# Kernel tuning notes

Hardware: AMD Instinct MI355X
Metric: run time of the kernel (lower is better)

Reference implementation:

```python
import jax, jax.numpy as jnp
import numpy as np

B, S1, S2, D1, D2, F = 8, 2048, 2048, 512, 512, 256

def setup_inputs() -> dict:
    key = jax.random.key(0)
    ks = jax.random.split(key, 10)
    sc1 = 1.0 / np.sqrt(D1)
    sc2 = 1.0 / np.sqrt(D2)
    scf = 1.0 / np.sqrt(F)
    return {
        "feat1": jax.random.normal(ks[0], (B, S1, D1), jnp.float32),
        "feat2": jax.random.normal(ks[1], (B, S2, D2), jnp.float32),
        "Wq": jax.random.normal(ks[2], (D1, F), jnp.float32) * sc1,
        "bq": jnp.zeros((F,), jnp.float32),
        "Wk": jax.random.normal(ks[3], (D2, F), jnp.float32) * sc2,
        "bk": jnp.zeros((F,), jnp.float32),
        "Wv": jax.random.normal(ks[4], (D2, F), jnp.float32) * sc2,
        "bv": jnp.zeros((F,), jnp.float32),
        "Wfc": jax.random.normal(ks[5], (F, F), jnp.float32) * scf,
        "bfc": jnp.zeros((F,), jnp.float32),
    }

def reference(feat1, feat2, Wq, bq, Wk, bk, Wv, bv, Wfc, bfc):
    Q = jnp.einsum('bsd,df->bsf', feat1, Wq) + bq          # [B,S1,F]
    K = jnp.einsum('btd,df->btf', feat2, Wk) + bk          # [B,S2,F]
    V = jnp.einsum('btd,df->btf', feat2, Wv) + bv          # [B,S2,F]
    scores = jnp.einsum('bsf,btf->bst', Q, K) / jnp.sqrt(jnp.float32(K.shape[-1]))
    attn = jax.nn.softmax(scores, axis=-1)                 # [B,S1,S2]
    attn_out = jnp.einsum('bst,btf->bsf', attn, V)         # [B,S1,F]
    out = jnp.einsum('bsf,fg->bsg', attn_out, Wfc) + bfc   # [B,S1,F]
    return out
```

## Files before the change

kernel.cpp:

```cpp
#include <hip/hip_runtime.h>
#include <hip/hip_bf16.h>

#define B_ 8
#define S1_ 2048
#define S2_ 2048
#define D_ 512
#define F_ 256

typedef __attribute__((ext_vector_type(4))) float f32x4;
typedef __attribute__((ext_vector_type(8))) short s16x8;
typedef __attribute__((ext_vector_type(4))) short s16x4;
typedef __attribute__((ext_vector_type(2))) int i32x2;

__device__ __forceinline__ short f2bf(float x) {
  union { float f; unsigned u; } v; v.f = x;
  unsigned r = v.u + 0x7fffu + ((v.u >> 16) & 1u);
  return (short)(r >> 16);
}

__device__ __forceinline__ int pk2bf(float a, float b) {
  union { __hip_bfloat162 h; int i; } u;
  u.h = __float22bfloat162_rn(make_float2(a, b));
  return u.i;
}

__global__ __launch_bounds__(256) void wtrans_kernel(
    const float* __restrict__ Wq, const float* __restrict__ Wk,
    const float* __restrict__ Wv, const float* __restrict__ Wfc,
    short* __restrict__ Wqt, short* __restrict__ Wkt,
    short* __restrict__ Wvt, short* __restrict__ Wfct) {
  int y = blockIdx.y;
  const float* W; short* Wt; int dl;
  if (y == 0)      { W = Wq;  Wt = Wqt;  dl = 9; }
  else if (y == 1) { W = Wk;  Wt = Wkt;  dl = 9; }
  else if (y == 2) { W = Wv;  Wt = Wvt;  dl = 9; }
  else             { W = Wfc; Wt = Wfct; dl = 8; }
  int idx = blockIdx.x * 256 + threadIdx.x;
  if (idx >= (F_ << dl)) return;
  int d = idx & ((1 << dl) - 1);
  int f = idx >> dl;
  Wt[idx] = f2bf(W[(size_t)d * F_ + f]);
}

__global__ __launch_bounds__(256) void proj_kernel(
    const float* __restrict__ feat1, const float* __restrict__ feat2,
    const short* __restrict__ Wqt, const short* __restrict__ Wkt,
    const short* __restrict__ Wvt,
    const float* __restrict__ bq, const float* __restrict__ bk,
    const float* __restrict__ bv,
    short* __restrict__ Qw, short* __restrict__ Kw, short* __restrict__ Vtw) {
  const float* A; const short* Wt; const float* bias; short* outp;
  float scale; int trans;
  if (blockIdx.z == 0)      { A = feat1; Wt = Wqt; bias = bq; outp = Qw;  scale = 0.0625f; trans = 0; }
  else if (blockIdx.z == 1) { A = feat2; Wt = Wkt; bias = bk; outp = Kw;  scale = 1.0f;    trans = 0; }
  else                      { A = feat2; Wt = Wvt; bias = bv; outp = Vtw; scale = 1.0f;    trans = 1; }

  __shared__ __align__(16) short As[128][72];
  __shared__ __align__(16) short Ws[128][72];

  int m0 = blockIdx.x * 128;
  int n0 = blockIdx.y * 128;
  int t = threadIdx.x;
  int w = t >> 6, L = t & 63, rowA = L & 15, quad = L >> 4;
  int wy = w >> 1, wx = w & 1;

  int srow = t >> 3, sc8 = (t & 7) * 8;

  f32x4 acc[4][4];
  for (int i = 0; i < 4; ++i)
    for (int j = 0; j < 4; ++j) acc[i][j] = (f32x4){0.f, 0.f, 0.f, 0.f};

  for (int k0 = 0; k0 < D_; k0 += 64) {
    for (int p = 0; p < 4; ++p) {
      int r = p * 32 + srow;
      const float* src = A + (size_t)(m0 + r) * D_ + k0 + sc8;
      f32x4 v0 = *(const f32x4*)src;
      f32x4 v1 = *(const f32x4*)(src + 4);
      s16x8 s;
      ((int*)&s)[0] = pk2bf(v0[0], v0[1]);
      ((int*)&s)[1] = pk2bf(v0[2], v0[3]);
      ((int*)&s)[2] = pk2bf(v1[0], v1[1]);
      ((int*)&s)[3] = pk2bf(v1[2], v1[3]);
      *(s16x8*)(&As[r][sc8]) = s;
    }
    for (int p = 0; p < 4; ++p) {
      int r = p * 32 + srow;
      *(s16x8*)(&Ws[r][sc8]) = *(const s16x8*)(Wt + (size_t)(n0 + r) * D_ + k0 + sc8);
    }
    __syncthreads();
    for (int kt = 0; kt < 2; ++kt) {
      s16x8 a[4];
      for (int mt = 0; mt < 4; ++mt)
        a[mt] = *(const s16x8*)(&As[wy * 64 + mt * 16 + rowA][kt * 32 + quad * 8]);
      for (int nt = 0; nt < 4; ++nt) {
        s16x8 b = *(const s16x8*)(&Ws[wx * 64 + nt * 16 + rowA][kt * 32 + quad * 8]);
        for (int mt = 0; mt < 4; ++mt)
          acc[mt][nt] = __builtin_amdgcn_mfma_f32_16x16x32_bf16(a[mt], b, acc[mt][nt], 0, 0, 0);
      }
    }
    __syncthreads();
  }

  if (!trans) {
    float bn[4];
    for (int nt = 0; nt < 4; ++nt) bn[nt] = bias[n0 + wx * 64 + nt * 16 + rowA];
    for (int mt = 0; mt < 4; ++mt) {
      int m = m0 + wy * 64 + mt * 16 + quad * 4;
      for (int nt = 0; nt < 4; ++nt) {
        int n = n0 + wx * 64 + nt * 16 + rowA;
        for (int r = 0; r < 4; ++r)
          outp[(size_t)(m + r) * F_ + n] = f2bf((acc[mt][nt][r] + bn[nt]) * scale);
      }
    }
  } else {
    int bb = m0 >> 11;
    int tbase = (m0 & (S2_ - 1)) + wy * 64;
    float bn[4];
    for (int nt = 0; nt < 4; ++nt) bn[nt] = bias[n0 + wx * 64 + nt * 16 + rowA];
    for (int nt = 0; nt < 4; ++nt) {
      int f = n0 + wx * 64 + nt * 16 + rowA;
      for (int mt = 0; mt < 4; ++mt) {
        int tt = tbase + mt * 16 + quad * 4;
        s16x4 o;
        for (int r = 0; r < 4; ++r) o[r] = f2bf(acc[mt][nt][r] + bn[nt]);
        *(s16x4*)(outp + ((size_t)bb * F_ + f) * S2_ + tt) = o;
      }
    }
  }
}

__global__ __launch_bounds__(512, 2) void flash_kernel(
    const short* __restrict__ Q,
    const short* __restrict__ K,
    const short* __restrict__ Vt,
    short* __restrict__ O) {
  __shared__ __align__(16) short Ks[2][64][264];
  __shared__ __align__(16) short Vs[2][256][72];
  __shared__ __align__(16) short Ps[4][16][72];

  int b = blockIdx.x >> 5;
  int s0 = (blockIdx.x & 31) * 64;
  int t = threadIdx.x;
  int w = t >> 6, L = t & 63, rowA = L & 15, quad = L >> 4;
  int rg = w & 3, ch = w >> 2;

  const short* Qb = Q + ((size_t)b * S1_ + s0 + rg * 16) * F_;
  const short* Kb = K + (size_t)b * S2_ * F_;
  const short* Vb = Vt + (size_t)b * F_ * S2_;

  int kr  = t >> 5;
  int kc8 = (t & 31) * 8;
  int vfb = t >> 3;
  int vc8 = (t & 7) * 8;

  s16x8 qf[8];
  for (int kt = 0; kt < 8; ++kt)
    qf[kt] = *(const s16x8*)(Qb + (size_t)rowA * F_ + kt * 32 + quad * 8);

  s16x8 kpre[4], vpre[4];
  for (int p = 0; p < 4; ++p) {
    kpre[p] = *(const s16x8*)(Kb + (size_t)(kr + p * 16) * F_ + kc8);
    vpre[p] = *(const s16x8*)(Vb + (size_t)(vfb + p * 64) * S2_ + vc8);
  }
  for (int p = 0; p < 4; ++p) {
    *(s16x8*)(&Ks[0][kr + p * 16][kc8]) = kpre[p];
    *(s16x8*)(&Vs[0][vfb + p * 64][vc8]) = vpre[p];
  }
  for (int p = 0; p < 4; ++p) {
    kpre[p] = *(const s16x8*)(Kb + (size_t)(64 + kr + p * 16) * F_ + kc8);
    vpre[p] = *(const s16x8*)(Vb + (size_t)(vfb + p * 64) * S2_ + 64 + vc8);
  }

  f32x4 o[8];
  for (int i = 0; i < 8; ++i) o[i] = (f32x4){0.f, 0.f, 0.f, 0.f};
  float l_lane[4] = {0.f, 0.f, 0.f, 0.f};

  for (int it = 0; it < 32; ++it) {
    int cb = it & 1;
    __syncthreads();
    if (it < 31) {
      for (int p = 0; p < 4; ++p) {
        *(s16x8*)(&Ks[1 - cb][kr + p * 16][kc8]) = kpre[p];
        *(s16x8*)(&Vs[1 - cb][vfb + p * 64][vc8]) = vpre[p];
      }
    }
    f32x4 s[2];
    s[0] = (f32x4){0.f, 0.f, 0.f, 0.f};
    s[1] = (f32x4){0.f, 0.f, 0.f, 0.f};
    for (int kt = 0; kt < 8; ++kt) {
      for (int n2 = 0; n2 < 2; ++n2) {
        s16x8 bfr = *(const s16x8*)(&Ks[cb][ch * 32 + n2 * 16 + rowA][kt * 32 + quad * 8]);
        s[n2] = __builtin_amdgcn_mfma_f32_16x16x32_bf16(qf[kt], bfr, s[n2], 0, 0, 0);
      }
    }
    for (int n2 = 0; n2 < 2; ++n2) {
      for (int r = 0; r < 4; ++r) {
        float p = __expf(s[n2][r]);
        l_lane[r] += p;
        Ps[rg][quad * 4 + r][ch * 32 + n2 * 16 + rowA] = f2bf(p);
      }
    }
    __syncthreads();
    if (it < 30) {
      int n0 = (it + 2) * 64;
      for (int p = 0; p < 4; ++p) {
        kpre[p] = *(const s16x8*)(Kb + (size_t)(n0 + kr + p * 16) * F_ + kc8);
        vpre[p] = *(const s16x8*)(Vb + (size_t)(vfb + p * 64) * S2_ + n0 + vc8);
      }
    }
    s16x8 pa0 = *(const s16x8*)(&Ps[rg][rowA][quad * 8]);
    s16x8 pa1 = *(const s16x8*)(&Ps[rg][rowA][32 + quad * 8]);
    for (int ft = 0; ft < 8; ++ft) {
      s16x8 v0 = *(const s16x8*)(&Vs[cb][ch * 128 + ft * 16 + rowA][quad * 8]);
      o[ft] = __builtin_amdgcn_mfma_f32_16x16x32_bf16(pa0, v0, o[ft], 0, 0, 0);
    }
    for (int ft = 0; ft < 8; ++ft) {
      s16x8 v1 = *(const s16x8*)(&Vs[cb][ch * 128 + ft * 16 + rowA][32 + quad * 8]);
      o[ft] = __builtin_amdgcn_mfma_f32_16x16x32_bf16(pa1, v1, o[ft], 0, 0, 0);
    }
  }

  float l[4];
  for (int r = 0; r < 4; ++r) {
    float x = l_lane[r];
    for (int off = 1; off < 16; off <<= 1)
      x += __shfl_xor(x, off, 64);
    l[r] = x;
  }
  __syncthreads();
  float* lf = (float*)&Ps[0][0][0];
  if (rowA == 0) {
    for (int r = 0; r < 4; ++r)
      lf[(rg * 16 + quad * 4 + r) * 2 + ch] = l[r];
  }
  __syncthreads();
  short* Ob = O + ((size_t)b * S1_ + s0 + rg * 16) * F_;
  for (int r = 0; r < 4; ++r) {
    int row = quad * 4 + r;
    float inv = 1.0f / (lf[(rg * 16 + row) * 2] + lf[(rg * 16 + row) * 2 + 1]);
    for (int ft = 0; ft < 8; ++ft)
      Ob[(size_t)row * F_ + ch * 128 + ft * 16 + rowA] = f2bf(o[ft][r] * inv);
  }
}

__global__ __launch_bounds__(256) void fc_kernel(
    const short* __restrict__ AO,
    const short* __restrict__ Wt,
    const float* __restrict__ bias,
    float* __restrict__ out) {
  __shared__ __align__(16) short As[128][72];
  __shared__ __align__(16) short Ws[128][72];

  int m0 = blockIdx.x * 128;
  int n0 = blockIdx.y * 128;
  int t = threadIdx.x;
  int w = t >> 6, L = t & 63, rowA = L & 15, quad = L >> 4;
  int wy = w >> 1, wx = w & 1;
  int srow = t >> 3, sc8 = (t & 7) * 8;

  f32x4 acc[4][4];
  for (int i = 0; i < 4; ++i)
    for (int j = 0; j < 4; ++j) acc[i][j] = (f32x4){0.f, 0.f, 0.f, 0.f};

  for (int k0 = 0; k0 < F_; k0 += 64) {
    for (int p = 0; p < 4; ++p) {
      int r = p * 32 + srow;
      *(s16x8*)(&As[r][sc8]) = *(const s16x8*)(AO + (size_t)(m0 + r) * F_ + k0 + sc8);
      *(s16x8*)(&Ws[r][sc8]) = *(const s16x8*)(Wt + (size_t)(n0 + r) * F_ + k0 + sc8);
    }
    __syncthreads();
    for (int kt = 0; kt < 2; ++kt) {
      s16x8 a[4];
      for (int mt = 0; mt < 4; ++mt)
        a[mt] = *(const s16x8*)(&As[wy * 64 + mt * 16 + rowA][kt * 32 + quad * 8]);
      for (int nt = 0; nt < 4; ++nt) {
        s16x8 b = *(const s16x8*)(&Ws[wx * 64 + nt * 16 + rowA][kt * 32 + quad * 8]);
        for (int mt = 0; mt < 4; ++mt)
          acc[mt][nt] = __builtin_amdgcn_mfma_f32_16x16x32_bf16(a[mt], b, acc[mt][nt], 0, 0, 0);
      }
    }
    __syncthreads();
  }

  float bn[4];
  for (int nt = 0; nt < 4; ++nt) bn[nt] = bias[n0 + wx * 64 + nt * 16 + rowA];
  for (int mt = 0; mt < 4; ++mt) {
    int m = m0 + wy * 64 + mt * 16 + quad * 4;
    for (int nt = 0; nt < 4; ++nt) {
      int n = n0 + wx * 64 + nt * 16 + rowA;
      for (int r = 0; r < 4; ++r)
        out[(size_t)(m + r) * F_ + n] = acc[mt][nt][r] + bn[nt];
    }
  }
}

extern "C" void kernel_launch(void* const* d_in, const int* in_sizes, int n_in,
                              void* d_out, int out_size, void* d_ws, size_t ws_size,
                              hipStream_t stream) {
  const float* feat1 = (const float*)d_in[0];
  const float* feat2 = (const float*)d_in[1];
  const float* Wq  = (const float*)d_in[2];
  const float* bq  = (const float*)d_in[3];
  const float* Wk  = (const float*)d_in[4];
  const float* bk  = (const float*)d_in[5];
  const float* Wv  = (const float*)d_in[6];
  const float* bv  = (const float*)d_in[7];
  const float* Wfc = (const float*)d_in[8];
  const float* bfc = (const float*)d_in[9];
  float* out = (float*)d_out;
  char* ws = (char*)d_ws;

  short* Qw   = (short*)(ws);
  short* Kw   = (short*)(ws + (size_t)(8u  << 20));
  short* Vtw  = (short*)(ws + (size_t)(16u << 20));
  short* AOw  = (short*)(ws + (size_t)(24u << 20));
  short* Wqt  = (short*)(ws + (size_t)(32u << 20));
  short* Wkt  = Wqt + 256 * 512;
  short* Wvt  = Wkt + 256 * 512;
  short* Wfct = Wvt + 256 * 512;

  wtrans_kernel<<<dim3(512, 4), 256, 0, stream>>>(Wq, Wk, Wv, Wfc, Wqt, Wkt, Wvt, Wfct);
  proj_kernel<<<dim3(128, 2, 3), 256, 0, stream>>>(feat1, feat2, Wqt, Wkt, Wvt,
                                                   bq, bk, bv, Qw, Kw, Vtw);
  flash_kernel<<<dim3(256), 512, 0, stream>>>(Qw, Kw, Vtw, AOw);
  fc_kernel<<<dim3(128, 2), 256, 0, stream>>>(AOw, Wfct, bfc, out);
}
```

Baseline: 220.0 us.

## Warp-specialize flash attention into score and PV waves; widen projection tiles

The flash kernel now splits its 8 waves into two roles. Four waves compute QK^T scores and the exp, writing P into a double-buffered shared tile. The other four waves do the P·V MFMAs one iteration behind, so score and output work overlap across the pipeline. K and V prefetch is restaged to match. Separately, the projection kernel uses 64x256 tiles so each block covers all of F and converts every fp32 activation row to bf16 only once, at the cost of a larger W tile in shared memory.

```diff
diff --git a/kernel.cpp b/kernel.cpp
--- a/kernel.cpp
+++ b/kernel.cpp
@@ -42,7 +42,7 @@
   Wt[idx] = f2bf(W[(size_t)d * F_ + f]);
 }
 
-__global__ __launch_bounds__(256) void proj_kernel(
+__global__ __launch_bounds__(256, 3) void proj_kernel(
     const float* __restrict__ feat1, const float* __restrict__ feat2,
     const short* __restrict__ Wqt, const short* __restrict__ Wkt,
     const short* __restrict__ Wvt,
@@ -51,51 +51,52 @@
     short* __restrict__ Qw, short* __restrict__ Kw, short* __restrict__ Vtw) {
   const float* A; const short* Wt; const float* bias; short* outp;
   float scale; int trans;
-  if (blockIdx.z == 0)      { A = feat1; Wt = Wqt; bias = bq; outp = Qw;  scale = 0.0625f; trans = 0; }
-  else if (blockIdx.z == 1) { A = feat2; Wt = Wkt; bias = bk; outp = Kw;  scale = 1.0f;    trans = 0; }
+  if (blockIdx.y == 0)      { A = feat1; Wt = Wqt; bias = bq; outp = Qw;  scale = 0.0625f; trans = 0; }
+  else if (blockIdx.y == 1) { A = feat2; Wt = Wkt; bias = bk; outp = Kw;  scale = 1.0f;    trans = 0; }
   else                      { A = feat2; Wt = Wvt; bias = bv; outp = Vtw; scale = 1.0f;    trans = 1; }
 
-  __shared__ __align__(16) short As[128][72];
-  __shared__ __align__(16) short Ws[128][72];
-
-  int m0 = blockIdx.x * 128;
-  int n0 = blockIdx.y * 128;
+  __shared__ __align__(16) short As[64][72];
+  __shared__ __align__(16) short Ws[256][72];
+
+  int m0 = blockIdx.x * 64;
   int t = threadIdx.x;
   int w = t >> 6, L = t & 63, rowA = L & 15, quad = L >> 4;
-  int wy = w >> 1, wx = w & 1;
-
-  int srow = t >> 3, sc8 = (t & 7) * 8;
+  int ar = t >> 2, ac16 = (t & 3) * 16;
 
   f32x4 acc[4][4];
   for (int i = 0; i < 4; ++i)
     for (int j = 0; j < 4; ++j) acc[i][j] = (f32x4){0.f, 0.f, 0.f, 0.f};
 
   for (int k0 = 0; k0 < D_; k0 += 64) {
+    {
+      const float* src = A + (size_t)(m0 + ar) * D_ + k0 + ac16;
+      f32x4 v0 = *(const f32x4*)(src);
+      f32x4 v1 = *(const f32x4*)(src + 4);
+      f32x4 v2 = *(const f32x4*)(src + 8);
+      f32x4 v3 = *(const f32x4*)(src + 12);
+      s16x8 s0, s1;
+      ((int*)&s0)[0] = pk2bf(v0[0], v0[1]); ((int*)&s0)[1] = pk2bf(v0[2], v0[3]);
+      ((int*)&s0)[2] = pk2bf(v1[0], v1[1]); ((int*)&s0)[3] = pk2bf(v1[2], v1[3]);
+      ((int*)&s1)[0] = pk2bf(v2[0], v2[1]); ((int*)&s1)[1] = pk2bf(v2[2], v2[3]);
+      ((int*)&s1)[2] = pk2bf(v3[0], v3[1]); ((int*)&s1)[3] = pk2bf(v3[2], v3[3]);
+      *(s16x8*)(&As[ar][ac16]) = s0;
+      *(s16x8*)(&As[ar][ac16 + 8]) = s1;
+    }
     for (int p = 0; p < 4; ++p) {
-      int r = p * 32 + srow;
-      const float* src = A + (size_t)(m0 + r) * D_ + k0 + sc8;
-      f32x4 v0 = *(const f32x4*)src;
-      f32x4 v1 = *(const f32x4*)(src + 4);
-      s16x8 s;
-      ((int*)&s)[0] = pk2bf(v0[0], v0[1]);
-      ((int*)&s)[1] = pk2bf(v0[2], v0[3]);
-      ((int*)&s)[2] = pk2bf(v1[0], v1[1]);
-      ((int*)&s)[3] = pk2bf(v1[2], v1[3]);
-      *(s16x8*)(&As[r][sc8]) = s;
-    }
-    for (int p = 0; p < 4; ++p) {
-      int r = p * 32 + srow;
-      *(s16x8*)(&Ws[r][sc8]) = *(const s16x8*)(Wt + (size_t)(n0 + r) * D_ + k0 + sc8);
+      int r = (t >> 2) + p * 64;
+      const short* src = Wt + (size_t)r * D_ + k0 + ac16;
+      *(s16x8*)(&Ws[r][ac16]) = *(const s16x8*)(src);
+      *(s16x8*)(&Ws[r][ac16 + 8]) = *(const s16x8*)(src + 8);
     }
     __syncthreads();
     for (int kt = 0; kt < 2; ++kt) {
       s16x8 a[4];
       for (int mt = 0; mt < 4; ++mt)
-        a[mt] = *(const s16x8*)(&As[wy * 64 + mt * 16 + rowA][kt * 32 + quad * 8]);
+        a[mt] = *(const s16x8*)(&As[mt * 16 + rowA][kt * 32 + quad * 8]);
       for (int nt = 0; nt < 4; ++nt) {
-        s16x8 b = *(const s16x8*)(&Ws[wx * 64 + nt * 16 + rowA][kt * 32 + quad * 8]);
+        s16x8 bfr = *(const s16x8*)(&Ws[w * 64 + nt * 16 + rowA][kt * 32 + quad * 8]);
         for (int mt = 0; mt < 4; ++mt)
-          acc[mt][nt] = __builtin_amdgcn_mfma_f32_16x16x32_bf16(a[mt], b, acc[mt][nt], 0, 0, 0);
+          acc[mt][nt] = __builtin_amdgcn_mfma_f32_16x16x32_bf16(a[mt], bfr, acc[mt][nt], 0, 0, 0);
       }
     }
     __syncthreads();
@@ -103,22 +104,22 @@
 
   if (!trans) {
     float bn[4];
-    for (int nt = 0; nt < 4; ++nt) bn[nt] = bias[n0 + wx * 64 + nt * 16 + rowA];
+    for (int nt = 0; nt < 4; ++nt) bn[nt] = bias[w * 64 + nt * 16 + rowA];
     for (int mt = 0; mt < 4; ++mt) {
-      int m = m0 + wy * 64 + mt * 16 + quad * 4;
+      int m = m0 + mt * 16 + quad * 4;
       for (int nt = 0; nt < 4; ++nt) {
-        int n = n0 + wx * 64 + nt * 16 + rowA;
+        int n = w * 64 + nt * 16 + rowA;
         for (int r = 0; r < 4; ++r)
           outp[(size_t)(m + r) * F_ + n] = f2bf((acc[mt][nt][r] + bn[nt]) * scale);
       }
     }
   } else {
     int bb = m0 >> 11;
-    int tbase = (m0 & (S2_ - 1)) + wy * 64;
+    int tbase = m0 & (S2_ - 1);
     float bn[4];
-    for (int nt = 0; nt < 4; ++nt) bn[nt] = bias[n0 + wx * 64 + nt * 16 + rowA];
+    for (int nt = 0; nt < 4; ++nt) bn[nt] = bias[w * 64 + nt * 16 + rowA];
     for (int nt = 0; nt < 4; ++nt) {
-      int f = n0 + wx * 64 + nt * 16 + rowA;
+      int f = w * 64 + nt * 16 + rowA;
       for (int mt = 0; mt < 4; ++mt) {
         int tt = tbase + mt * 16 + quad * 4;
         s16x4 o;
@@ -136,110 +137,123 @@
     short* __restrict__ O) {
   __shared__ __align__(16) short Ks[2][64][264];
   __shared__ __align__(16) short Vs[2][256][72];
-  __shared__ __align__(16) short Ps[4][16][72];
+  __shared__ __align__(16) short Ps[2][64][72];
 
   int b = blockIdx.x >> 5;
   int s0 = (blockIdx.x & 31) * 64;
   int t = threadIdx.x;
   int w = t >> 6, L = t & 63, rowA = L & 15, quad = L >> 4;
-  int rg = w & 3, ch = w >> 2;
-
-  const short* Qb = Q + ((size_t)b * S1_ + s0 + rg * 16) * F_;
+  int isS = (w < 4);
+
   const short* Kb = K + (size_t)b * S2_ * F_;
   const short* Vb = Vt + (size_t)b * F_ * S2_;
 
-  int kr  = t >> 5;
-  int kc8 = (t & 31) * 8;
-  int vfb = t >> 3;
-  int vc8 = (t & 7) * 8;
-
-  s16x8 qf[8];
-  for (int kt = 0; kt < 8; ++kt)
-    qf[kt] = *(const s16x8*)(Qb + (size_t)rowA * F_ + kt * 32 + quad * 8);
+  int kr = t >> 5, kc8 = (t & 31) * 8;
+  int vr = t >> 3, vc8 = (t & 7) * 8;
+
+  int rs = (w & 1) * 32, cs = ((w >> 1) & 1) * 32;
+  int mg = (w - 4) & 1, fg = ((w - 4) >> 1) & 1;
+
+  s16x8 qf[2][8];
+  if (isS) {
+    const short* Qb = Q + ((size_t)b * S1_ + s0 + rs) * F_;
+    for (int mt = 0; mt < 2; ++mt)
+      for (int kt = 0; kt < 8; ++kt)
+        qf[mt][kt] = *(const s16x8*)(Qb + (size_t)(mt * 16 + rowA) * F_ + kt * 32 + quad * 8);
+  }
+  f32x4 o[2][8];
+  for (int i = 0; i < 2; ++i)
+    for (int j = 0; j < 8; ++j) o[i][j] = (f32x4){0.f, 0.f, 0.f, 0.f};
+  float l_lane[2][4] = {{0.f,0.f,0.f,0.f},{0.f,0.f,0.f,0.f}};
 
   s16x8 kpre[4], vpre[4];
-  for (int p = 0; p < 4; ++p) {
+  for (int p = 0; p < 4; ++p)
     kpre[p] = *(const s16x8*)(Kb + (size_t)(kr + p * 16) * F_ + kc8);
-    vpre[p] = *(const s16x8*)(Vb + (size_t)(vfb + p * 64) * S2_ + vc8);
-  }
-  for (int p = 0; p < 4; ++p) {
+  for (int p = 0; p < 4; ++p)
     *(s16x8*)(&Ks[0][kr + p * 16][kc8]) = kpre[p];
-    *(s16x8*)(&Vs[0][vfb + p * 64][vc8]) = vpre[p];
-  }
-  for (int p = 0; p < 4; ++p) {
+  for (int p = 0; p < 4; ++p)
     kpre[p] = *(const s16x8*)(Kb + (size_t)(64 + kr + p * 16) * F_ + kc8);
-    vpre[p] = *(const s16x8*)(Vb + (size_t)(vfb + p * 64) * S2_ + 64 + vc8);
-  }
-
-  f32x4 o[8];
-  for (int i = 0; i < 8; ++i) o[i] = (f32x4){0.f, 0.f, 0.f, 0.f};
-  float l_lane[4] = {0.f, 0.f, 0.f, 0.f};
-
-  for (int it = 0; it < 32; ++it) {
+  for (int p = 0; p < 4; ++p)
+    vpre[p] = *(const s16x8*)(Vb + (size_t)(vr + p * 64) * S2_ + vc8);
+
+  for (int it = 0; it <= 32; ++it) {
     int cb = it & 1;
     __syncthreads();
-    if (it < 31) {
-      for (int p = 0; p < 4; ++p) {
-        *(s16x8*)(&Ks[1 - cb][kr + p * 16][kc8]) = kpre[p];
-        *(s16x8*)(&Vs[1 - cb][vfb + p * 64][vc8]) = vpre[p];
-      }
-    }
-    f32x4 s[2];
-    s[0] = (f32x4){0.f, 0.f, 0.f, 0.f};
-    s[1] = (f32x4){0.f, 0.f, 0.f, 0.f};
-    for (int kt = 0; kt < 8; ++kt) {
-      for (int n2 = 0; n2 < 2; ++n2) {
-        s16x8 bfr = *(const s16x8*)(&Ks[cb][ch * 32 + n2 * 16 + rowA][kt * 32 + quad * 8]);
-        s[n2] = __builtin_amdgcn_mfma_f32_16x16x32_bf16(qf[kt], bfr, s[n2], 0, 0, 0);
-      }
-    }
-    for (int n2 = 0; n2 < 2; ++n2) {
+    if (it < 32) {
+      for (int p = 0; p < 4; ++p)
+        *(s16x8*)(&Vs[cb][vr + p * 64][vc8]) = vpre[p];
+      if (it < 31) {
+        for (int p = 0; p < 4; ++p)
+          *(s16x8*)(&Ks[1 - cb][kr + p * 16][kc8]) = kpre[p];
+        int n0 = (it + 1) * 64;
+        for (int p = 0; p < 4; ++p)
+          vpre[p] = *(const s16x8*)(Vb + (size_t)(vr + p * 64) * S2_ + n0 + vc8);
+      }
+      if (it < 30) {
+        int n0 = (it + 2) * 64;
+        for (int p = 0; p < 4; ++p)
+          kpre[p] = *(const s16x8*)(Kb + (size_t)(n0 + kr + p * 16) * F_ + kc8);
+      }
+    }
+    if (isS) {
+      if (it < 32) {
+        f32x4 s[2][2];
+        for (int i = 0; i < 2; ++i)
+          for (int j = 0; j < 2; ++j) s[i][j] = (f32x4){0.f, 0.f, 0.f, 0.f};
+        for (int kt = 0; kt < 8; ++kt) {
+          s16x8 bf0 = *(const s16x8*)(&Ks[cb][cs + rowA][kt * 32 + quad * 8]);
+          s16x8 bf1 = *(const s16x8*)(&Ks[cb][cs + 16 + rowA][kt * 32 + quad * 8]);
+          for (int mt = 0; mt < 2; ++mt) {
+            s[mt][0] = __builtin_amdgcn_mfma_f32_16x16x32_bf16(qf[mt][kt], bf0, s[mt][0], 0, 0, 0);
+            s[mt][1] = __builtin_amdgcn_mfma_f32_16x16x32_bf16(qf[mt][kt], bf1, s[mt][1], 0, 0, 0);
+          }
+        }
+        for (int mt = 0; mt < 2; ++mt)
+          for (int nt = 0; nt < 2; ++nt)
+            for (int r = 0; r < 4; ++r) {
+              float p = __expf(s[mt][nt][r]);
+              l_lane[mt][r] += p;
+              Ps[cb][rs + mt * 16 + quad * 4 + r][cs + nt * 16 + rowA] = f2bf(p);
+            }
+      }
+    } else {
+      if (it > 0) {
+        int pb = 1 - cb;
+        s16x8 pa[2][2];
+        for (int mt = 0; mt < 2; ++mt)
+          for (int kt = 0; kt < 2; ++kt)
+            pa[mt][kt] = *(const s16x8*)(&Ps[pb][mg * 32 + mt * 16 + rowA][kt * 32 + quad * 8]);
+        for (int ft = 0; ft < 8; ++ft)
+          for (int kt = 0; kt < 2; ++kt) {
+            s16x8 vf = *(const s16x8*)(&Vs[pb][fg * 128 + ft * 16 + rowA][kt * 32 + quad * 8]);
+            for (int mt = 0; mt < 2; ++mt)
+              o[mt][ft] = __builtin_amdgcn_mfma_f32_16x16x32_bf16(pa[mt][kt], vf, o[mt][ft], 0, 0, 0);
+          }
+      }
+    }
+  }
+
+  float* lf = (float*)&Ks[0][0][0];
+  if (isS) {
+    for (int mt = 0; mt < 2; ++mt)
       for (int r = 0; r < 4; ++r) {
-        float p = __expf(s[n2][r]);
-        l_lane[r] += p;
-        Ps[rg][quad * 4 + r][ch * 32 + n2 * 16 + rowA] = f2bf(p);
-      }
-    }
-    __syncthreads();
-    if (it < 30) {
-      int n0 = (it + 2) * 64;
-      for (int p = 0; p < 4; ++p) {
-        kpre[p] = *(const s16x8*)(Kb + (size_t)(n0 + kr + p * 16) * F_ + kc8);
-        vpre[p] = *(const s16x8*)(Vb + (size_t)(vfb + p * 64) * S2_ + n0 + vc8);
-      }
-    }
-    s16x8 pa0 = *(const s16x8*)(&Ps[rg][rowA][quad * 8]);
-    s16x8 pa1 = *(const s16x8*)(&Ps[rg][rowA][32 + quad * 8]);
-    for (int ft = 0; ft < 8; ++ft) {
-      s16x8 v0 = *(const s16x8*)(&Vs[cb][ch * 128 + ft * 16 + rowA][quad * 8]);
-      o[ft] = __builtin_amdgcn_mfma_f32_16x16x32_bf16(pa0, v0, o[ft], 0, 0, 0);
-    }
-    for (int ft = 0; ft < 8; ++ft) {
-      s16x8 v1 = *(const s16x8*)(&Vs[cb][ch * 128 + ft * 16 + rowA][32 + quad * 8]);
-      o[ft] = __builtin_amdgcn_mfma_f32_16x16x32_bf16(pa1, v1, o[ft], 0, 0, 0);
-    }
-  }
-
-  float l[4];
-  for (int r = 0; r < 4; ++r) {
-    float x = l_lane[r];
-    for (int off = 1; off < 16; off <<= 1)
-      x += __shfl_xor(x, off, 64);
-    l[r] = x;
+        float x = l_lane[mt][r];
+        for (int off = 1; off < 16; off <<= 1)
+          x += __shfl_xor(x, off, 64);
+        if (rowA == 0)
+          lf[((w >> 1) & 1) * 64 + rs + mt * 16 + quad * 4 + r] = x;
+      }
   }
   __syncthreads();
-  float* lf = (float*)&Ps[0][0][0];
-  if (rowA == 0) {
-    for (int r = 0; r < 4; ++r)
-      lf[(rg * 16 + quad * 4 + r) * 2 + ch] = l[r];
-  }
-  __syncthreads();
-  short* Ob = O + ((size_t)b * S1_ + s0 + rg * 16) * F_;
-  for (int r = 0; r < 4; ++r) {
-    int row = quad * 4 + r;
-    float inv = 1.0f / (lf[(rg * 16 + row) * 2] + lf[(rg * 16 + row) * 2 + 1]);
-    for (int ft = 0; ft < 8; ++ft)
-      Ob[(size_t)row * F_ + ch * 128 + ft * 16 + rowA] = f2bf(o[ft][r] * inv);
+  if (!isS) {
+    short* Ob = O + ((size_t)b * S1_ + s0) * F_;
+    for (int mt = 0; mt < 2; ++mt)
+      for (int r = 0; r < 4; ++r) {
+        int row = mg * 32 + mt * 16 + quad * 4 + r;
+        float inv = 1.0f / (lf[row] + lf[64 + row]);
+        for (int ft = 0; ft < 8; ++ft)
+          Ob[(size_t)row * F_ + fg * 128 + ft * 16 + rowA] = f2bf(o[mt][ft][r] * inv);
+      }
   }
 }
 
@@ -274,9 +288,9 @@
       for (int mt = 0; mt < 4; ++mt)
         a[mt] = *(const s16x8*)(&As[wy * 64 + mt * 16 + rowA][kt * 32 + quad * 8]);
       for (int nt = 0; nt < 4; ++nt) {
-        s16x8 b = *(const s16x8*)(&Ws[wx * 64 + nt * 16 + rowA][kt * 32 + quad * 8]);
+        s16x8 bfr = *(const s16x8*)(&Ws[wx * 64 + nt * 16 + rowA][kt * 32 + quad * 8]);
         for (int mt = 0; mt < 4; ++mt)
-          acc[mt][nt] = __builtin_amdgcn_mfma_f32_16x16x32_bf16(a[mt], b, acc[mt][nt], 0, 0, 0);
+          acc[mt][nt] = __builtin_amdgcn_mfma_f32_16x16x32_bf16(a[mt], bfr, acc[mt][nt], 0, 0, 0);
       }
     }
     __syncthreads();
@@ -320,8 +334,8 @@
   short* Wfct = Wvt + 256 * 512;
 
   wtrans_kernel<<<dim3(512, 4), 256, 0, stream>>>(Wq, Wk, Wv, Wfc, Wqt, Wkt, Wvt, Wfct);
-  proj_kernel<<<dim3(128, 2, 3), 256, 0, stream>>>(feat1, feat2, Wqt, Wkt, Wvt,
-                                                   bq, bk, bv, Qw, Kw, Vtw);
+  proj_kernel<<<dim3(256, 3), 256, 0, stream>>>(feat1, feat2, Wqt, Wkt, Wvt,
+                                                bq, bk, bv, Qw, Kw, Vtw);
   flash_kernel<<<dim3(256), 512, 0, stream>>>(Qw, Kw, Vtw, AOw);
   fc_kernel<<<dim3(128, 2), 256, 0, stream>>>(AOw, Wfct, bfc, out);
 }
```

Measured after the change: 195.5 us. 11.1% less time.
